# Performance work log

Hardware: AMD Instinct MI355X
Metric: run time of the kernel (lower is better)

## Reference

```python
import jax, jax.numpy as jnp
import numpy as np

N, E, DIN, DOUT, NB = 50000, 800000, 64, 64, 16
MAX_RADIUS = 10.0


def setup_inputs() -> dict:
    key = jax.random.key(0)
    ks = jax.random.split(key, 16)
    x = jax.random.normal(ks[0], (N, DIN), dtype=jnp.float32)
    edge_index = jax.random.randint(ks[1], (2, E), 0, N, dtype=jnp.int64)
    edge_vec = jax.random.normal(ks[2], (E, 3), dtype=jnp.float32)
    edge_len = jax.random.uniform(ks[3], (E, 1), dtype=jnp.float32) * MAX_RADIUS
    def lin(k, fan_in, fan_out):
        b = 1.0 / np.sqrt(fan_in)
        kw, kb = jax.random.split(k)
        W = jax.random.uniform(kw, (fan_in, fan_out), minval=-b, maxval=b, dtype=jnp.float32)
        bias = jax.random.uniform(kb, (fan_out,), minval=-b, maxval=b, dtype=jnp.float32)
        return W, bias
    mw1, mb1 = lin(ks[4], 2 * DIN + NB, 2 * DOUT)
    mw2, mb2 = lin(ks[5], 2 * DOUT, DOUT)
    uw1, ub1 = lin(ks[6], DIN + DOUT, DOUT)
    uw2, ub2 = lin(ks[7], DOUT, DOUT)
    ln_g = jnp.ones((DOUT,), dtype=jnp.float32)
    ln_b = jnp.zeros((DOUT,), dtype=jnp.float32)
    return {"x": x, "edge_index": edge_index, "edge_vec": edge_vec, "edge_len": edge_len,
            "mw1": mw1, "mb1": mb1, "mw2": mw2, "mb2": mb2,
            "uw1": uw1, "ub1": ub1, "uw2": uw2, "ub2": ub2,
            "ln_g": ln_g, "ln_b": ln_b}


def reference(x, edge_index, edge_vec, edge_len,
              mw1, mb1, mw2, mb2, uw1, ub1, uw2, ub2, ln_g, ln_b):
    src, dst = edge_index[0], edge_index[1]
    # Gaussian RBF expansion of edge lengths (fallback path hardcodes 16 bases)
    dist = edge_len[:, 0]                                # [E]
    centers = jnp.linspace(0.0, MAX_RADIUS, NB)          # [NB]
    width = (centers[1] - centers[0]) * 0.5
    rbf = jnp.exp(-((dist[:, None] - centers) ** 2) / (2.0 * width ** 2))  # [E,NB]
    # message MLP over gathered node pairs
    msg_in = jnp.concatenate([x[src], x[dst], rbf], axis=-1)  # [E, 2*DIN+NB]
    msg = jax.nn.silu(msg_in @ mw1 + mb1) @ mw2 + mb2         # [E, DOUT]
    # mean aggregation via scatter-add (counts clamped to >=1)
    agg = jax.ops.segment_sum(msg, dst, num_segments=x.shape[0])           # [N, DOUT]
    cnt = jax.ops.segment_sum(jnp.ones((dst.shape[0],), dtype=x.dtype), dst,
                              num_segments=x.shape[0])                     # [N]
    agg = agg / jnp.maximum(cnt, 1.0)[:, None]
    # update MLP + LayerNorm
    upd_in = jnp.concatenate([x, agg], axis=-1)                # [N, DIN+DOUT]
    out = jax.nn.silu(upd_in @ uw1 + ub1) @ uw2 + ub2          # [N, DOUT]
    mu = out.mean(-1, keepdims=True)
    var = ((out - mu) ** 2).mean(-1, keepdims=True)
    out = (out - mu) * jax.lax.rsqrt(var + 1e-5) * ln_g + ln_b
    return out
```

## Files before the change

### kernel.cpp

```cpp
#include <hip/hip_runtime.h>
#include <cstdint>

#define NN 50000
#define NE 800000
#define NT 12500
#define NBLK 1792
#define MSW 168
#define HSW 136
#define UPS 136
#define HBS 72

typedef short short8 __attribute__((ext_vector_type(8)));
typedef float f32x4  __attribute__((ext_vector_type(4)));

__device__ __forceinline__ ushort f2bf(float f) {
    union { float f; uint u; } v; v.f = f;
    return (ushort)((v.u + 0x7FFFu + ((v.u >> 16) & 1u)) >> 16);
}
__device__ __forceinline__ float silu(float v) {
    return __fdividef(v, 1.0f + __expf(-v));
}

__global__ __launch_bounds__(256) void conv_x_hist(const float* __restrict__ x,
                                                   const int* __restrict__ ei,
                                                   ushort* __restrict__ xb,
                                                   int* __restrict__ h2) {
    int i = blockIdx.x * 256 + threadIdx.x;
    float4 v = ((const float4*)x)[i];
    uint2 o;
    o.x = (uint)f2bf(v.x) | ((uint)f2bf(v.y) << 16);
    o.y = (uint)f2bf(v.z) | ((uint)f2bf(v.w) << 16);
    ((uint2*)xb)[i] = o;
    atomicAdd(&h2[(blockIdx.x & 7) * NN + ei[NE + i]], 1);
}

__global__ __launch_bounds__(256) void conv_w(const float* __restrict__ mw1,
                                              const float* __restrict__ mw2,
                                              const float* __restrict__ uw1,
                                              const float* __restrict__ uw2,
                                              ushort* __restrict__ w1t,
                                              ushort* __restrict__ w2t,
                                              ushort* __restrict__ uw1t,
                                              ushort* __restrict__ uw2t) {
    int i = blockIdx.x * 256 + threadIdx.x;
    if (i < 20480) {
        int h = i / 160, k = i % 160;
        w1t[i] = f2bf(k < 144 ? mw1[k * 128 + h] : 0.0f);
    } else if (i < 28672) {
        int j = i - 20480, o = j / 128, k = j % 128;
        w2t[j] = f2bf(mw2[k * 64 + o]);
    } else if (i < 36864) {
        int j = i - 28672, o = j / 128, k = j % 128;
        uw1t[j] = f2bf(uw1[k * 64 + o]);
    } else {
        int j = i - 36864, o = j / 64, k = j % 64;
        uw2t[j] = f2bf(uw2[k * 64 + o]);
    }
}

__global__ __launch_bounds__(256) void scan1(const int* __restrict__ h2,
                                             int* __restrict__ hist_comb,
                                             int* __restrict__ starts,
                                             int* __restrict__ bsum) {
    __shared__ int s[256];
    int t = threadIdx.x, b = blockIdx.x, i = b * 256 + t;
    int v = 0;
    if (i < NN) {
        #pragma unroll
        for (int xg = 0; xg < 8; ++xg) v += h2[xg * NN + i];
        hist_comb[i] = v;
    }
    s[t] = v; __syncthreads();
    #pragma unroll
    for (int off = 1; off < 256; off <<= 1) {
        int a = (t >= off) ? s[t - off] : 0;
        __syncthreads();
        s[t] += a;
        __syncthreads();
    }
    if (i < NN) starts[i] = s[t] - v;
    if (t == 255) bsum[b] = s[255];
}

__global__ __launch_bounds__(256) void scan2(int* __restrict__ bsum) {
    __shared__ int s[256];
    int t = threadIdx.x;
    int v = (t < 196) ? bsum[t] : 0;
    s[t] = v; __syncthreads();
    #pragma unroll
    for (int off = 1; off < 256; off <<= 1) {
        int a = (t >= off) ? s[t - off] : 0;
        __syncthreads();
        s[t] += a;
        __syncthreads();
    }
    if (t < 196) bsum[t] = s[t] - v;
}

__global__ __launch_bounds__(256) void cursor_init(const int* __restrict__ starts,
                                                   const int* __restrict__ bsum,
                                                   const int* __restrict__ h2,
                                                   int* __restrict__ cursor2) {
    int d = blockIdx.x * 256 + threadIdx.x;
    if (d < NN) {
        int c = starts[d] + bsum[blockIdx.x];
        #pragma unroll
        for (int xg = 0; xg < 8; ++xg) {
            cursor2[xg * NN + d] = c;
            c += h2[xg * NN + d];
        }
    }
}

__global__ __launch_bounds__(256) void rank_k(const int* __restrict__ ei,
                                              const float* __restrict__ elen,
                                              int* __restrict__ cursor2,
                                              uint* __restrict__ ssdp,
                                              float* __restrict__ selen) {
    int e = blockIdx.x * 256 + threadIdx.x;
    int sN = ei[e];
    int d  = ei[NE + e];
    float L = elen[e];
    int pos = atomicAdd(&cursor2[(blockIdx.x & 7) * NN + d], 1);
    ssdp[pos]  = (uint)sN | ((uint)d << 16);
    selen[pos] = L;
}

__global__ __launch_bounds__(256, 4) void edge_mfma(
    const ushort* __restrict__ xb,
    const uint*   __restrict__ ssdp,
    const float*  __restrict__ selen,
    const ushort* __restrict__ w1t,
    const float*  __restrict__ mb1,
    const ushort* __restrict__ w2t,
    const float*  __restrict__ mb2,
    float* __restrict__ agg)
{
    __shared__ ushort buf[64 * MSW];

    const int tid  = threadIdx.x;
    const int wv   = tid >> 6;
    const int lane = tid & 63;
    const int l16  = lane & 15;
    const int g    = lane >> 4;

    short8 a1[2][5];
    #pragma unroll
    for (int m = 0; m < 2; ++m)
        #pragma unroll
        for (int kk = 0; kk < 5; ++kk)
            a1[m][kk] = *(const short8*)(w1t + (wv*32 + m*16 + l16)*160 + kk*32 + g*8);
    short8 a2[4];
    #pragma unroll
    for (int kk = 0; kk < 4; ++kk)
        a2[kk] = *(const short8*)(w2t + (wv*16 + l16)*128 + kk*32 + g*8);
    float b1v[2][4], b2v[4];
    #pragma unroll
    for (int m = 0; m < 2; ++m)
        #pragma unroll
        for (int r = 0; r < 4; ++r)
            b1v[m][r] = mb1[wv*32 + m*16 + g*4 + r];
    #pragma unroll
    for (int r = 0; r < 4; ++r)
        b2v[r] = mb2[wv*16 + g*4 + r];

    const int q  = NT / NBLK, r = NT % NBLK;
    const int t0 = blockIdx.x < r ? blockIdx.x * (q + 1)
                                  : r * (q + 1) + (blockIdx.x - r) * q;
    const int tn = blockIdx.x < r ? q + 1 : q;

    const int ea = tid >> 3, cc = tid & 7;

    {
        const int e0 = t0 * 64;
        uint sda = ssdp[e0 + ea], sdb = ssdp[e0 + 32 + ea];
        float ela = selen[e0 + ea], elb = selen[e0 + 32 + ea];
        *(uint4*)&buf[ ea       *MSW      + cc*8] = *(const uint4*)(xb + (size_t)(sda & 0xFFFFu)*64 + cc*8);
        *(uint4*)&buf[(32 + ea) *MSW      + cc*8] = *(const uint4*)(xb + (size_t)(sdb & 0xFFFFu)*64 + cc*8);
        *(uint4*)&buf[ ea       *MSW + 64 + cc*8] = *(const uint4*)(xb + (size_t)(sda >> 16)*64 + cc*8);
        *(uint4*)&buf[(32 + ea) *MSW + 64 + cc*8] = *(const uint4*)(xb + (size_t)(sdb >> 16)*64 + cc*8);
        float u0 = ela - (float)(2*cc)   * (10.0f/15.0f);
        float u1 = ela - (float)(2*cc+1) * (10.0f/15.0f);
        *(uint*)&buf[ea*MSW + 128 + cc*2] =
            (uint)f2bf(__expf(-u0*u0*4.5f)) | ((uint)f2bf(__expf(-u1*u1*4.5f)) << 16);
        float v0 = elb - (float)(2*cc)   * (10.0f/15.0f);
        float v1 = elb - (float)(2*cc+1) * (10.0f/15.0f);
        *(uint*)&buf[(32+ea)*MSW + 128 + cc*2] =
            (uint)f2bf(__expf(-v0*v0*4.5f)) | ((uint)f2bf(__expf(-v1*v1*4.5f)) << 16);
        int ez = tid >> 2, qq = tid & 3;
        *(uint2*)&buf[ez*MSW + 144 + qq*4] = make_uint2(0u, 0u);
    }
    int dvals[4];
    #pragma unroll
    for (int nt = 0; nt < 4; ++nt)
        dvals[nt] = (int)(ssdp[t0*64 + nt*16 + l16] >> 16);

    for (int tt = 0; tt < tn; ++tt) {
        __syncthreads();

        const bool hn = (tt + 1 < tn);
        const int e1 = (t0 + tt + 1) * 64;
        uint4 pf0, pf1, pf2, pf3; float pea = 0.f, peb = 0.f; int pdv[4];
        if (hn) {
            uint sda = ssdp[e1 + ea], sdb = ssdp[e1 + 32 + ea];
            pea = selen[e1 + ea]; peb = selen[e1 + 32 + ea];
            pf0 = *(const uint4*)(xb + (size_t)(sda & 0xFFFFu)*64 + cc*8);
            pf1 = *(const uint4*)(xb + (size_t)(sdb & 0xFFFFu)*64 + cc*8);
            pf2 = *(const uint4*)(xb + (size_t)(sda >> 16)*64 + cc*8);
            pf3 = *(const uint4*)(xb + (size_t)(sdb >> 16)*64 + cc*8);
            #pragma unroll
            for (int nt = 0; nt < 4; ++nt)
                pdv[nt] = (int)(ssdp[e1 + nt*16 + l16] >> 16);
        }

        f32x4 c1[2][4];
        #pragma unroll
        for (int m = 0; m < 2; ++m)
            #pragma unroll
            for (int nt = 0; nt < 4; ++nt)
                c1[m][nt] = (f32x4){b1v[m][0], b1v[m][1], b1v[m][2], b1v[m][3]};
        #pragma unroll
        for (int nt = 0; nt < 4; ++nt)
            #pragma unroll
            for (int kk = 0; kk < 5; ++kk) {
                short8 b = *(const short8*)&buf[(nt*16 + l16)*MSW + kk*32 + g*8];
                c1[0][nt] = __builtin_amdgcn_mfma_f32_16x16x32_bf16(a1[0][kk], b, c1[0][nt], 0, 0, 0);
                c1[1][nt] = __builtin_amdgcn_mfma_f32_16x16x32_bf16(a1[1][kk], b, c1[1][nt], 0, 0, 0);
            }
        __syncthreads();

        #pragma unroll
        for (int m = 0; m < 2; ++m)
            #pragma unroll
            for (int nt = 0; nt < 4; ++nt) {
                uint2 pk;
                pk.x = (uint)f2bf(silu(c1[m][nt][0])) | ((uint)f2bf(silu(c1[m][nt][1])) << 16);
                pk.y = (uint)f2bf(silu(c1[m][nt][2])) | ((uint)f2bf(silu(c1[m][nt][3])) << 16);
                *(uint2*)&buf[(nt*16 + l16)*HSW + wv*32 + m*16 + g*4] = pk;
            }
        __syncthreads();

        f32x4 c2[4];
        #pragma unroll
        for (int nt = 0; nt < 4; ++nt)
            c2[nt] = (f32x4){b2v[0], b2v[1], b2v[2], b2v[3]};
        #pragma unroll
        for (int nt = 0; nt < 4; ++nt)
            #pragma unroll
            for (int kk = 0; kk < 4; ++kk) {
                short8 b = *(const short8*)&buf[(nt*16 + l16)*HSW + kk*32 + g*8];
                c2[nt] = __builtin_amdgcn_mfma_f32_16x16x32_bf16(a2[kk], b, c2[nt], 0, 0, 0);
            }

        #pragma unroll
        for (int nt = 0; nt < 4; ++nt) {
            int d  = dvals[nt];
            int dp = __shfl_up(d, 1, 16);
            int f  = (l16 == 0 || d != dp) ? 1 : 0;
            float v0 = c2[nt][0], v1 = c2[nt][1], v2 = c2[nt][2], v3 = c2[nt][3];
            #pragma unroll
            for (int off = 1; off < 16; off <<= 1) {
                float w0 = __shfl_up(v0, off, 16);
                float w1 = __shfl_up(v1, off, 16);
                float w2 = __shfl_up(v2, off, 16);
                float w3 = __shfl_up(v3, off, 16);
                int   ff = __shfl_up(f,  off, 16);
                if (l16 >= off && !f) { v0 += w0; v1 += w1; v2 += w2; v3 += w3; }
                if (l16 >= off) f |= ff;
            }
            int dn = __shfl_down(d, 1, 16);
            if (l16 == 15 || d != dn) {
                float* p = agg + (size_t)d * 64 + wv * 16 + g * 4;
                atomicAdd(p + 0, v0);
                atomicAdd(p + 1, v1);
                atomicAdd(p + 2, v2);
                atomicAdd(p + 3, v3);
            }
        }
        __syncthreads();

        if (hn) {
            *(uint4*)&buf[ ea       *MSW      + cc*8] = pf0;
            *(uint4*)&buf[(32 + ea) *MSW      + cc*8] = pf1;
            *(uint4*)&buf[ ea       *MSW + 64 + cc*8] = pf2;
            *(uint4*)&buf[(32 + ea) *MSW + 64 + cc*8] = pf3;
            float u0 = pea - (float)(2*cc)   * (10.0f/15.0f);
            float u1 = pea - (float)(2*cc+1) * (10.0f/15.0f);
            *(uint*)&buf[ea*MSW + 128 + cc*2] =
                (uint)f2bf(__expf(-u0*u0*4.5f)) | ((uint)f2bf(__expf(-u1*u1*4.5f)) << 16);
            float v0 = peb - (float)(2*cc)   * (10.0f/15.0f);
            float v1 = peb - (float)(2*cc+1) * (10.0f/15.0f);
            *(uint*)&buf[(32+ea)*MSW + 128 + cc*2] =
                (uint)f2bf(__expf(-v0*v0*4.5f)) | ((uint)f2bf(__expf(-v1*v1*4.5f)) << 16);
            int ez = tid >> 2, qq = tid & 3;
            *(uint2*)&buf[ez*MSW + 144 + qq*4] = make_uint2(0u, 0u);
            #pragma unroll
            for (int nt = 0; nt < 4; ++nt) dvals[nt] = pdv[nt];
        }
    }
}

__global__ __launch_bounds__(256, 4) void node_mfma(
    const ushort* __restrict__ xb,
    const float*  __restrict__ agg,
    const int*    __restrict__ hist,
    const ushort* __restrict__ uw1t,
    const float*  __restrict__ ub1,
    const ushort* __restrict__ uw2t,
    const float*  __restrict__ ub2,
    const float*  __restrict__ lng,
    const float*  __restrict__ lnb,
    float* __restrict__ out)
{
    __shared__ ushort upd_s[64 * UPS];
    __shared__ ushort hb_s[64 * HBS];

    const int tid  = threadIdx.x;
    const int wv   = tid >> 6;
    const int lane = tid & 63;
    const int l16  = lane & 15;
    const int g    = lane >> 4;
    const int nb   = blockIdx.x * 64;

    short8 au1[4];
    #pragma unroll
    for (int kk = 0; kk < 4; ++kk)
        au1[kk] = *(const short8*)(uw1t + (wv*16 + l16)*128 + kk*32 + g*8);
    short8 au2[4][2];
    #pragma unroll
    for (int m = 0; m < 4; ++m)
        #pragma unroll
        for (int kk = 0; kk < 2; ++kk)
            au2[m][kk] = *(const short8*)(uw2t + (m*16 + l16)*64 + kk*32 + g*8);
    float bu1[4];
    #pragma unroll
    for (int rr = 0; rr < 4; ++rr)
        bu1[rr] = ub1[wv*16 + g*4 + rr];

    #pragma unroll
    for (int i = 0; i < 2; ++i) {
        int idx = i * 256 + tid, nd = (idx >> 3) & 63, cg = idx & 7;
        int n = nb + nd;
        uint4 v = make_uint4(0u, 0u, 0u, 0u);
        if (n < NN) v = *(const uint4*)(xb + (size_t)n * 64 + cg * 8);
        *(uint4*)&upd_s[nd * UPS + cg * 8] = v;
    }
    {
        int nd = tid >> 2, c16 = (tid & 3) * 16;
        int n = nb + nd;
        float rc = 0.0f;
        if (n < NN) rc = 1.0f / fmaxf((float)hist[n], 1.0f);
        const float4* ap = (const float4*)(agg + (size_t)(n < NN ? n : 0) * 64 + c16);
        #pragma unroll
        for (int j = 0; j < 4; ++j) {
            float4 v = (n < NN) ? ap[j] : make_float4(0.f, 0.f, 0.f, 0.f);
            uint2 pk;
            pk.x = (uint)f2bf(v.x * rc) | ((uint)f2bf(v.y * rc) << 16);
            pk.y = (uint)f2bf(v.z * rc) | ((uint)f2bf(v.w * rc) << 16);
            *(uint2*)&upd_s[nd * UPS + 64 + c16 + j * 4] = pk;
        }
    }
    __syncthreads();

    f32x4 c1[4];
    #pragma unroll
    for (int nt = 0; nt < 4; ++nt)
        c1[nt] = (f32x4){bu1[0], bu1[1], bu1[2], bu1[3]};
    #pragma unroll
    for (int nt = 0; nt < 4; ++nt)
        #pragma unroll
        for (int kk = 0; kk < 4; ++kk) {
            short8 b = *(const short8*)&upd_s[(nt*16 + l16)*UPS + kk*32 + g*8];
            c1[nt] = __builtin_amdgcn_mfma_f32_16x16x32_bf16(au1[kk], b, c1[nt], 0, 0, 0);
        }
    #pragma unroll
    for (int nt = 0; nt < 4; ++nt) {
        uint2 pk;
        pk.x = (uint)f2bf(silu(c1[nt][0])) | ((uint)f2bf(silu(c1[nt][1])) << 16);
        pk.y = (uint)f2bf(silu(c1[nt][2])) | ((uint)f2bf(silu(c1[nt][3])) << 16);
        *(uint2*)&hb_s[(nt*16 + l16)*HBS + wv*16 + g*4] = pk;
    }
    __syncthreads();

    short8 fb[2];
    #pragma unroll
    for (int kk = 0; kk < 2; ++kk)
        fb[kk] = *(const short8*)&hb_s[(wv*16 + l16)*HBS + kk*32 + g*8];
    f32x4 c2[4];
    #pragma unroll
    for (int m = 0; m < 4; ++m) {
        c2[m] = *(const f32x4*)&ub2[m*16 + g*4];
        #pragma unroll
        for (int kk = 0; kk < 2; ++kk)
            c2[m] = __builtin_amdgcn_mfma_f32_16x16x32_bf16(au2[m][kk], fb[kk], c2[m], 0, 0, 0);
    }

    float s = 0.0f;
    #pragma unroll
    for (int m = 0; m < 4; ++m)
        #pragma unroll
        for (int rr = 0; rr < 4; ++rr) s += c2[m][rr];
    s += __shfl_xor(s, 16); s += __shfl_xor(s, 32);
    float mu = s * (1.0f / 64.0f);
    float sq = 0.0f;
    #pragma unroll
    for (int m = 0; m < 4; ++m)
        #pragma unroll
        for (int rr = 0; rr < 4; ++rr) {
            float dd = c2[m][rr] - mu; sq += dd * dd;
        }
    sq += __shfl_xor(sq, 16); sq += __shfl_xor(sq, 32);
    float rst = rsqrtf(sq * (1.0f / 64.0f) + 1e-5f);

    int n = nb + wv*16 + l16;
    if (n < NN) {
        #pragma unroll
        for (int m = 0; m < 4; ++m) {
            f32x4 g4 = *(const f32x4*)&lng[m*16 + g*4];
            f32x4 b4 = *(const f32x4*)&lnb[m*16 + g*4];
            f32x4 o;
            #pragma unroll
            for (int rr = 0; rr < 4; ++rr)
                o[rr] = (c2[m][rr] - mu) * rst * g4[rr] + b4[rr];
            *(f32x4*)&out[(size_t)n * 64 + m*16 + g*4] = o;
        }
    }
}

extern "C" void kernel_launch(void* const* d_in, const int* in_sizes, int n_in,
                              void* d_out, int out_size, void* d_ws, size_t ws_size,
                              hipStream_t stream) {
    const float* x    = (const float*)d_in[0];
    const int*   ei   = (const int*)  d_in[1];
    const float* elen = (const float*)d_in[3];
    const float* mw1  = (const float*)d_in[4];
    const float* mb1  = (const float*)d_in[5];
    const float* mw2  = (const float*)d_in[6];
    const float* mb2  = (const float*)d_in[7];
    const float* uw1  = (const float*)d_in[8];
    const float* ub1  = (const float*)d_in[9];
    const float* uw2  = (const float*)d_in[10];
    const float* ub2  = (const float*)d_in[11];
    const float* lng  = (const float*)d_in[12];
    const float* lnb  = (const float*)d_in[13];

    char*  ws        = (char*)d_ws;
    float* agg       = (float*)ws;
    int*   h2        = (int*)(ws + 0);
    int*   starts    = (int*)(ws + 1600000);
    int*   bsum      = (int*)(ws + 1800000);
    int*   cursor2   = (int*)(ws + 1900000);
    int*   hist_comb = (int*)(ws + 12800000);
    uint*  ssdp      = (uint*)(ws + 13000000);
    float* selen     = (float*)(ws + 16200000);
    ushort* xb   = (ushort*)(ws + 19400000);
    ushort* w1t  = (ushort*)(ws + 25800000);
    ushort* w2t  = (ushort*)(ws + 25840960);
    ushort* uw1t = (ushort*)(ws + 25857344);
    ushort* uw2t = (ushort*)(ws + 25873728);

    hipMemsetAsync(h2, 0, 1600000, stream);
    conv_x_hist<<<3125, 256, 0, stream>>>(x, ei, xb, h2);
    conv_w<<<160, 256, 0, stream>>>(mw1, mw2, uw1, uw2, w1t, w2t, uw1t, uw2t);
    scan1<<<196, 256, 0, stream>>>(h2, hist_comb, starts, bsum);
    scan2<<<1, 256, 0, stream>>>(bsum);
    cursor_init<<<196, 256, 0, stream>>>(starts, bsum, h2, cursor2);
    rank_k<<<3125, 256, 0, stream>>>(ei, elen, cursor2, ssdp, selen);
    hipMemsetAsync(agg, 0, 12800000, stream);
    edge_mfma<<<NBLK, 256, 0, stream>>>(xb, ssdp, selen, w1t, mb1, w2t, mb2, agg);
    node_mfma<<<782, 256, 0, stream>>>(xb, agg, hist_comb, uw1t, ub1, uw2t, ub2,
                                       lng, lnb, (float*)d_out);
}
```

Measured before the change: 363.3 us.

## Double-buffer edge tile staging, pack edge records, and fuse setup kernels

The edge MLP kernel now uses two shared-memory tile buffers. The next tile's gathered features and RBF values are written to the alternate buffer while the current tile's atomics run, which removes one block barrier per tile. Source/destination and edge length are packed into one uint2 record so each edge needs a single load. Two setup kernel pairs are merged: x/weight conversion, and scan2 into cursor_init, where every block redoes the small scan. Shared memory doubles, and the launch bound drops to 3 blocks per CU, which lowers occupancy.

```diff
diff --git a/kernel.cpp b/kernel.cpp
--- a/kernel.cpp
+++ b/kernel.cpp
@@ -21,40 +21,42 @@
     return __fdividef(v, 1.0f + __expf(-v));
 }
 
-__global__ __launch_bounds__(256) void conv_x_hist(const float* __restrict__ x,
-                                                   const int* __restrict__ ei,
-                                                   ushort* __restrict__ xb,
-                                                   int* __restrict__ h2) {
-    int i = blockIdx.x * 256 + threadIdx.x;
-    float4 v = ((const float4*)x)[i];
-    uint2 o;
-    o.x = (uint)f2bf(v.x) | ((uint)f2bf(v.y) << 16);
-    o.y = (uint)f2bf(v.z) | ((uint)f2bf(v.w) << 16);
-    ((uint2*)xb)[i] = o;
-    atomicAdd(&h2[(blockIdx.x & 7) * NN + ei[NE + i]], 1);
-}
-
-__global__ __launch_bounds__(256) void conv_w(const float* __restrict__ mw1,
-                                              const float* __restrict__ mw2,
-                                              const float* __restrict__ uw1,
-                                              const float* __restrict__ uw2,
-                                              ushort* __restrict__ w1t,
-                                              ushort* __restrict__ w2t,
-                                              ushort* __restrict__ uw1t,
-                                              ushort* __restrict__ uw2t) {
-    int i = blockIdx.x * 256 + threadIdx.x;
-    if (i < 20480) {
-        int h = i / 160, k = i % 160;
-        w1t[i] = f2bf(k < 144 ? mw1[k * 128 + h] : 0.0f);
-    } else if (i < 28672) {
-        int j = i - 20480, o = j / 128, k = j % 128;
-        w2t[j] = f2bf(mw2[k * 64 + o]);
-    } else if (i < 36864) {
-        int j = i - 28672, o = j / 128, k = j % 128;
-        uw1t[j] = f2bf(uw1[k * 64 + o]);
+__global__ __launch_bounds__(256) void conv_fused(const float* __restrict__ x,
+                                                  const int* __restrict__ ei,
+                                                  const float* __restrict__ mw1,
+                                                  const float* __restrict__ mw2,
+                                                  const float* __restrict__ uw1,
+                                                  const float* __restrict__ uw2,
+                                                  ushort* __restrict__ xb,
+                                                  int* __restrict__ h2,
+                                                  ushort* __restrict__ w1t,
+                                                  ushort* __restrict__ w2t,
+                                                  ushort* __restrict__ uw1t,
+                                                  ushort* __restrict__ uw2t) {
+    int b = blockIdx.x;
+    if (b < 3125) {
+        int i = b * 256 + threadIdx.x;
+        float4 v = ((const float4*)x)[i];
+        uint2 o;
+        o.x = (uint)f2bf(v.x) | ((uint)f2bf(v.y) << 16);
+        o.y = (uint)f2bf(v.z) | ((uint)f2bf(v.w) << 16);
+        ((uint2*)xb)[i] = o;
+        atomicAdd(&h2[(b & 7) * NN + ei[NE + i]], 1);
     } else {
-        int j = i - 36864, o = j / 64, k = j % 64;
-        uw2t[j] = f2bf(uw2[k * 64 + o]);
+        int i = (b - 3125) * 256 + threadIdx.x;
+        if (i < 20480) {
+            int h = i / 160, k = i % 160;
+            w1t[i] = f2bf(k < 144 ? mw1[k * 128 + h] : 0.0f);
+        } else if (i < 28672) {
+            int j = i - 20480, o = j / 128, k = j % 128;
+            w2t[j] = f2bf(mw2[k * 64 + o]);
+        } else if (i < 36864) {
+            int j = i - 28672, o = j / 128, k = j % 128;
+            uw1t[j] = f2bf(uw1[k * 64 + o]);
+        } else {
+            int j = i - 36864, o = j / 64, k = j % 64;
+            uw2t[j] = f2bf(uw2[k * 64 + o]);
+        }
     }
 }
 
@@ -82,28 +84,25 @@
     if (t == 255) bsum[b] = s[255];
 }
 
-__global__ __launch_bounds__(256) void scan2(int* __restrict__ bsum) {
-    __shared__ int s[256];
-    int t = threadIdx.x;
-    int v = (t < 196) ? bsum[t] : 0;
-    s[t] = v; __syncthreads();
-    #pragma unroll
-    for (int off = 1; off < 256; off <<= 1) {
-        int a = (t >= off) ? s[t - off] : 0;
-        __syncthreads();
-        s[t] += a;
-        __syncthreads();
-    }
-    if (t < 196) bsum[t] = s[t] - v;
-}
-
 __global__ __launch_bounds__(256) void cursor_init(const int* __restrict__ starts,
                                                    const int* __restrict__ bsum,
                                                    const int* __restrict__ h2,
                                                    int* __restrict__ cursor2) {
-    int d = blockIdx.x * 256 + threadIdx.x;
+    __shared__ int sb[256];
+    int t = threadIdx.x;
+    int v = (t < 196) ? bsum[t] : 0;
+    sb[t] = v; __syncthreads();
+    #pragma unroll
+    for (int off = 1; off < 256; off <<= 1) {
+        int a = (t >= off) ? sb[t - off] : 0;
+        __syncthreads();
+        sb[t] += a;
+        __syncthreads();
+    }
+    int base = (blockIdx.x == 0) ? 0 : sb[blockIdx.x - 1];
+    int d = blockIdx.x * 256 + t;
     if (d < NN) {
-        int c = starts[d] + bsum[blockIdx.x];
+        int c = starts[d] + base;
         #pragma unroll
         for (int xg = 0; xg < 8; ++xg) {
             cursor2[xg * NN + d] = c;
@@ -115,28 +114,25 @@
 __global__ __launch_bounds__(256) void rank_k(const int* __restrict__ ei,
                                               const float* __restrict__ elen,
                                               int* __restrict__ cursor2,
-                                              uint* __restrict__ ssdp,
-                                              float* __restrict__ selen) {
+                                              uint2* __restrict__ ssde) {
     int e = blockIdx.x * 256 + threadIdx.x;
     int sN = ei[e];
     int d  = ei[NE + e];
     float L = elen[e];
     int pos = atomicAdd(&cursor2[(blockIdx.x & 7) * NN + d], 1);
-    ssdp[pos]  = (uint)sN | ((uint)d << 16);
-    selen[pos] = L;
-}
-
-__global__ __launch_bounds__(256, 4) void edge_mfma(
+    ssde[pos] = make_uint2((uint)sN | ((uint)d << 16), __float_as_uint(L));
+}
+
+__global__ __launch_bounds__(256, 3) void edge_mfma(
     const ushort* __restrict__ xb,
-    const uint*   __restrict__ ssdp,
-    const float*  __restrict__ selen,
+    const uint2*  __restrict__ ssde,
     const ushort* __restrict__ w1t,
     const float*  __restrict__ mb1,
     const ushort* __restrict__ w2t,
     const float*  __restrict__ mb2,
     float* __restrict__ agg)
 {
-    __shared__ ushort buf[64 * MSW];
+    __shared__ ushort buf[2][64 * MSW];
 
     const int tid  = threadIdx.x;
     const int wv   = tid >> 6;
@@ -170,47 +166,47 @@
     const int tn = blockIdx.x < r ? q + 1 : q;
 
     const int ea = tid >> 3, cc = tid & 7;
+    const int ez = tid >> 2, qq = tid & 3;
 
     {
         const int e0 = t0 * 64;
-        uint sda = ssdp[e0 + ea], sdb = ssdp[e0 + 32 + ea];
-        float ela = selen[e0 + ea], elb = selen[e0 + 32 + ea];
-        *(uint4*)&buf[ ea       *MSW      + cc*8] = *(const uint4*)(xb + (size_t)(sda & 0xFFFFu)*64 + cc*8);
-        *(uint4*)&buf[(32 + ea) *MSW      + cc*8] = *(const uint4*)(xb + (size_t)(sdb & 0xFFFFu)*64 + cc*8);
-        *(uint4*)&buf[ ea       *MSW + 64 + cc*8] = *(const uint4*)(xb + (size_t)(sda >> 16)*64 + cc*8);
-        *(uint4*)&buf[(32 + ea) *MSW + 64 + cc*8] = *(const uint4*)(xb + (size_t)(sdb >> 16)*64 + cc*8);
+        uint2 sda = ssde[e0 + ea], sdb = ssde[e0 + 32 + ea];
+        float ela = __uint_as_float(sda.y), elb = __uint_as_float(sdb.y);
+        *(uint4*)&buf[0][ ea     *MSW      + cc*8] = *(const uint4*)(xb + (size_t)(sda.x & 0xFFFFu)*64 + cc*8);
+        *(uint4*)&buf[0][(32+ea)*MSW      + cc*8] = *(const uint4*)(xb + (size_t)(sdb.x & 0xFFFFu)*64 + cc*8);
+        *(uint4*)&buf[0][ ea     *MSW + 64 + cc*8] = *(const uint4*)(xb + (size_t)(sda.x >> 16)*64 + cc*8);
+        *(uint4*)&buf[0][(32+ea)*MSW + 64 + cc*8] = *(const uint4*)(xb + (size_t)(sdb.x >> 16)*64 + cc*8);
         float u0 = ela - (float)(2*cc)   * (10.0f/15.0f);
         float u1 = ela - (float)(2*cc+1) * (10.0f/15.0f);
-        *(uint*)&buf[ea*MSW + 128 + cc*2] =
+        *(uint*)&buf[0][ea*MSW + 128 + cc*2] =
             (uint)f2bf(__expf(-u0*u0*4.5f)) | ((uint)f2bf(__expf(-u1*u1*4.5f)) << 16);
         float v0 = elb - (float)(2*cc)   * (10.0f/15.0f);
         float v1 = elb - (float)(2*cc+1) * (10.0f/15.0f);
-        *(uint*)&buf[(32+ea)*MSW + 128 + cc*2] =
+        *(uint*)&buf[0][(32+ea)*MSW + 128 + cc*2] =
             (uint)f2bf(__expf(-v0*v0*4.5f)) | ((uint)f2bf(__expf(-v1*v1*4.5f)) << 16);
-        int ez = tid >> 2, qq = tid & 3;
-        *(uint2*)&buf[ez*MSW + 144 + qq*4] = make_uint2(0u, 0u);
+        *(uint2*)&buf[0][ez*MSW + 144 + qq*4] = make_uint2(0u, 0u);
     }
     int dvals[4];
     #pragma unroll
     for (int nt = 0; nt < 4; ++nt)
-        dvals[nt] = (int)(ssdp[t0*64 + nt*16 + l16] >> 16);
-
+        dvals[nt] = (int)(ssde[t0*64 + nt*16 + l16].x >> 16);
+
+    int cur = 0;
     for (int tt = 0; tt < tn; ++tt) {
         __syncthreads();
 
         const bool hn = (tt + 1 < tn);
         const int e1 = (t0 + tt + 1) * 64;
-        uint4 pf0, pf1, pf2, pf3; float pea = 0.f, peb = 0.f; int pdv[4];
+        uint4 pf0, pf1, pf2, pf3; uint2 psa, psb; int pdv[4];
         if (hn) {
-            uint sda = ssdp[e1 + ea], sdb = ssdp[e1 + 32 + ea];
-            pea = selen[e1 + ea]; peb = selen[e1 + 32 + ea];
-            pf0 = *(const uint4*)(xb + (size_t)(sda & 0xFFFFu)*64 + cc*8);
-            pf1 = *(const uint4*)(xb + (size_t)(sdb & 0xFFFFu)*64 + cc*8);
-            pf2 = *(const uint4*)(xb + (size_t)(sda >> 16)*64 + cc*8);
-            pf3 = *(const uint4*)(xb + (size_t)(sdb >> 16)*64 + cc*8);
+            psa = ssde[e1 + ea]; psb = ssde[e1 + 32 + ea];
+            pf0 = *(const uint4*)(xb + (size_t)(psa.x & 0xFFFFu)*64 + cc*8);
+            pf1 = *(const uint4*)(xb + (size_t)(psb.x & 0xFFFFu)*64 + cc*8);
+            pf2 = *(const uint4*)(xb + (size_t)(psa.x >> 16)*64 + cc*8);
+            pf3 = *(const uint4*)(xb + (size_t)(psb.x >> 16)*64 + cc*8);
             #pragma unroll
             for (int nt = 0; nt < 4; ++nt)
-                pdv[nt] = (int)(ssdp[e1 + nt*16 + l16] >> 16);
+                pdv[nt] = (int)(ssde[e1 + nt*16 + l16].x >> 16);
         }
 
         f32x4 c1[2][4];
@@ -223,7 +219,7 @@
         for (int nt = 0; nt < 4; ++nt)
             #pragma unroll
             for (int kk = 0; kk < 5; ++kk) {
-                short8 b = *(const short8*)&buf[(nt*16 + l16)*MSW + kk*32 + g*8];
+                short8 b = *(const short8*)&buf[cur][(nt*16 + l16)*MSW + kk*32 + g*8];
                 c1[0][nt] = __builtin_amdgcn_mfma_f32_16x16x32_bf16(a1[0][kk], b, c1[0][nt], 0, 0, 0);
                 c1[1][nt] = __builtin_amdgcn_mfma_f32_16x16x32_bf16(a1[1][kk], b, c1[1][nt], 0, 0, 0);
             }
@@ -236,7 +232,7 @@
                 uint2 pk;
                 pk.x = (uint)f2bf(silu(c1[m][nt][0])) | ((uint)f2bf(silu(c1[m][nt][1])) << 16);
                 pk.y = (uint)f2bf(silu(c1[m][nt][2])) | ((uint)f2bf(silu(c1[m][nt][3])) << 16);
-                *(uint2*)&buf[(nt*16 + l16)*HSW + wv*32 + m*16 + g*4] = pk;
+                *(uint2*)&buf[cur][(nt*16 + l16)*HSW + wv*32 + m*16 + g*4] = pk;
             }
         __syncthreads();
 
@@ -248,9 +244,27 @@
         for (int nt = 0; nt < 4; ++nt)
             #pragma unroll
             for (int kk = 0; kk < 4; ++kk) {
-                short8 b = *(const short8*)&buf[(nt*16 + l16)*HSW + kk*32 + g*8];
+                short8 b = *(const short8*)&buf[cur][(nt*16 + l16)*HSW + kk*32 + g*8];
                 c2[nt] = __builtin_amdgcn_mfma_f32_16x16x32_bf16(a2[kk], b, c2[nt], 0, 0, 0);
             }
+
+        if (hn) {
+            int al = cur ^ 1;
+            *(uint4*)&buf[al][ ea     *MSW      + cc*8] = pf0;
+            *(uint4*)&buf[al][(32+ea)*MSW      + cc*8] = pf1;
+            *(uint4*)&buf[al][ ea     *MSW + 64 + cc*8] = pf2;
+            *(uint4*)&buf[al][(32+ea)*MSW + 64 + cc*8] = pf3;
+            float pea = __uint_as_float(psa.y), peb = __uint_as_float(psb.y);
+            float u0 = pea - (float)(2*cc)   * (10.0f/15.0f);
+            float u1 = pea - (float)(2*cc+1) * (10.0f/15.0f);
+            *(uint*)&buf[al][ea*MSW + 128 + cc*2] =
+                (uint)f2bf(__expf(-u0*u0*4.5f)) | ((uint)f2bf(__expf(-u1*u1*4.5f)) << 16);
+            float v0 = peb - (float)(2*cc)   * (10.0f/15.0f);
+            float v1 = peb - (float)(2*cc+1) * (10.0f/15.0f);
+            *(uint*)&buf[al][(32+ea)*MSW + 128 + cc*2] =
+                (uint)f2bf(__expf(-v0*v0*4.5f)) | ((uint)f2bf(__expf(-v1*v1*4.5f)) << 16);
+            *(uint2*)&buf[al][ez*MSW + 144 + qq*4] = make_uint2(0u, 0u);
+        }
 
         #pragma unroll
         for (int nt = 0; nt < 4; ++nt) {
@@ -277,26 +291,12 @@
                 atomicAdd(p + 3, v3);
             }
         }
-        __syncthreads();
 
         if (hn) {
-            *(uint4*)&buf[ ea       *MSW      + cc*8] = pf0;
-            *(uint4*)&buf[(32 + ea) *MSW      + cc*8] = pf1;
-            *(uint4*)&buf[ ea       *MSW + 64 + cc*8] = pf2;
-            *(uint4*)&buf[(32 + ea) *MSW + 64 + cc*8] = pf3;
-            float u0 = pea - (float)(2*cc)   * (10.0f/15.0f);
-            float u1 = pea - (float)(2*cc+1) * (10.0f/15.0f);
-            *(uint*)&buf[ea*MSW + 128 + cc*2] =
-                (uint)f2bf(__expf(-u0*u0*4.5f)) | ((uint)f2bf(__expf(-u1*u1*4.5f)) << 16);
-            float v0 = peb - (float)(2*cc)   * (10.0f/15.0f);
-            float v1 = peb - (float)(2*cc+1) * (10.0f/15.0f);
-            *(uint*)&buf[(32+ea)*MSW + 128 + cc*2] =
-                (uint)f2bf(__expf(-v0*v0*4.5f)) | ((uint)f2bf(__expf(-v1*v1*4.5f)) << 16);
-            int ez = tid >> 2, qq = tid & 3;
-            *(uint2*)&buf[ez*MSW + 144 + qq*4] = make_uint2(0u, 0u);
             #pragma unroll
             for (int nt = 0; nt < 4; ++nt) dvals[nt] = pdv[nt];
         }
+        cur ^= 1;
     }
 }
 
@@ -451,8 +451,7 @@
     int*   bsum      = (int*)(ws + 1800000);
     int*   cursor2   = (int*)(ws + 1900000);
     int*   hist_comb = (int*)(ws + 12800000);
-    uint*  ssdp      = (uint*)(ws + 13000000);
-    float* selen     = (float*)(ws + 16200000);
+    uint2* ssde      = (uint2*)(ws + 13000000);
     ushort* xb   = (ushort*)(ws + 19400000);
     ushort* w1t  = (ushort*)(ws + 25800000);
     ushort* w2t  = (ushort*)(ws + 25840960);
@@ -460,14 +459,13 @@
     ushort* uw2t = (ushort*)(ws + 25873728);
 
     hipMemsetAsync(h2, 0, 1600000, stream);
-    conv_x_hist<<<3125, 256, 0, stream>>>(x, ei, xb, h2);
-    conv_w<<<160, 256, 0, stream>>>(mw1, mw2, uw1, uw2, w1t, w2t, uw1t, uw2t);
+    conv_fused<<<3285, 256, 0, stream>>>(x, ei, mw1, mw2, uw1, uw2,
+                                         xb, h2, w1t, w2t, uw1t, uw2t);
     scan1<<<196, 256, 0, stream>>>(h2, hist_comb, starts, bsum);
-    scan2<<<1, 256, 0, stream>>>(bsum);
     cursor_init<<<196, 256, 0, stream>>>(starts, bsum, h2, cursor2);
-    rank_k<<<3125, 256, 0, stream>>>(ei, elen, cursor2, ssdp, selen);
+    rank_k<<<3125, 256, 0, stream>>>(ei, elen, cursor2, ssde);
     hipMemsetAsync(agg, 0, 12800000, stream);
-    edge_mfma<<<NBLK, 256, 0, stream>>>(xb, ssdp, selen, w1t, mb1, w2t, mb2, agg);
+    edge_mfma<<<NBLK, 256, 0, stream>>>(xb, ssde, w1t, mb1, w2t, mb2, agg);
     node_mfma<<<782, 256, 0, stream>>>(xb, agg, hist_comb, uw1t, ub1, uw2t, ub2,
                                        lng, lnb, (float*)d_out);
 }
```

After: 336.4 us. -7.4%, faster.
